# Performance work log

Hardware: AMD Instinct MI355X
Metric: run time of the kernel (lower is better)

Reference implementation:

```python
import jax, jax.numpy as jnp
import numpy as np

B, C, H, W = 4, 256, 64, 64
C8 = C // 8


def setup_inputs() -> dict:
    key = jax.random.key(0)
    ks = jax.random.split(key, 10)
    return {
        "x": jax.random.normal(ks[0], (B, C, H, W), jnp.float32),
        "x_encoder": jax.random.normal(ks[1], (B, C, H, W), jnp.float32),
        "Wq": jax.random.normal(ks[2], (C8, C), jnp.float32) * 0.05,
        "bq": jax.random.normal(ks[3], (C8,), jnp.float32) * 0.05,
        "Wk": jax.random.normal(ks[4], (C8, C), jnp.float32) * 0.05,
        "bk": jax.random.normal(ks[5], (C8,), jnp.float32) * 0.05,
        "Wv": jax.random.normal(ks[6], (C, C), jnp.float32) * 0.05,
        "bv": jax.random.normal(ks[7], (C,), jnp.float32) * 0.05,
        "h_pos": jax.random.normal(ks[8], (1, C8, H, 1), jnp.float32),
        "w_pos": jax.random.normal(ks[9], (1, C8, 1, W), jnp.float32),
        "gamma": jnp.zeros((1,), jnp.float32),
    }


def reference(x, x_encoder, Wq, bq, Wk, bk, Wv, bv, h_pos, w_pos, gamma):
    b, c, h, w = x.shape
    n = h * w
    c8 = Wq.shape[0]
    # 1x1 convs are channel-wise matmuls over flattened spatial dim
    xf = x.reshape(b, c, n)            # [B, C, N]
    xe = x_encoder.reshape(b, c, n)    # [B, C, N]
    q = jnp.einsum("oc,bcn->bno", Wq, xf) + bq[None, None, :]   # [B, N, C8]
    k = jnp.einsum("oc,bcn->bon", Wk, xe) + bk[None, :, None]   # [B, C8, N]
    energy = jnp.einsum("bnc,bcm->bnm", q, k)                    # [B, N, N]
    pos = (h_pos + w_pos).reshape(c8, n)                         # [C8, N]
    energy = energy + jnp.einsum("bnc,cm->bnm", q, pos)
    attn = jax.nn.softmax(energy, axis=-1)                       # [B, N, N]
    v = jnp.einsum("oc,bcn->bon", Wv, xe) + bv[None, :, None]    # [B, C, N]
    out = jnp.einsum("bcm,bnm->bcn", v, attn).reshape(b, c, h, w)
    return gamma * out + x
```

## Files before the change

kernel.cpp:

```cpp
#include <hip/hip_runtime.h>
#include <hip/hip_bf16.h>
#include <math.h>

#define BB 4
#define CC 256
#define C8 32
#define HH 64
#define WW 64
#define NN 4096
#define QBLK 64
#define NT 32
#define LOG2E 1.44269504088896340736f

typedef __attribute__((ext_vector_type(8)))  short bh8;
typedef __attribute__((ext_vector_type(4)))  float f4;
typedef __attribute__((ext_vector_type(16))) float f16v;

#if __has_builtin(__builtin_amdgcn_exp2f)
#define EXP2(x) __builtin_amdgcn_exp2f(x)
#else
#define EXP2(x) exp2f(x)
#endif

static __device__ __forceinline__ unsigned short f2bf(float f) {
    union { float f; unsigned int u; } v; v.f = f;
    return (unsigned short)((v.u + 0x7FFFu + ((v.u >> 16) & 1u)) >> 16);
}

static __device__ __forceinline__ unsigned int cvtpk(float lo, float hi) {
    unsigned int r;
    asm("v_cvt_pk_bf16_f32 %0, %1, %2" : "=v"(r) : "v"(lo), "v"(hi));
    return r;
}

static __device__ __forceinline__ bh8 pack_frag(unsigned int w0, unsigned int w1,
                                                unsigned int w2, unsigned int w3) {
    union { unsigned int u[4]; bh8 v; } z;
    z.u[0] = w0; z.u[1] = w1; z.u[2] = w2; z.u[3] = w3;
    return z.v;
}

__global__ __launch_bounds__(256) void wconv_kernel(
    const float* __restrict__ Wq, const float* __restrict__ Wk,
    const float* __restrict__ Wv, unsigned short* __restrict__ wb)
{
    int f = (blockIdx.x * 256 + threadIdx.x) * 4;
    const float* src;
    if (f < 32 * 256)           src = Wq + f;
    else if (f < 64 * 256)      src = Wk + (f - 32 * 256);
    else                        src = Wv + (f - 64 * 256);
    float4 v = *reinterpret_cast<const float4*>(src);
    ushort4 o;
    o.x = f2bf(v.x); o.y = f2bf(v.y); o.z = f2bf(v.z); o.w = f2bf(v.w);
    *reinterpret_cast<ushort4*>(wb + f) = o;
}

__global__ __launch_bounds__(640, 1) void proj_kernel(
    const float* __restrict__ x, const float* __restrict__ xe,
    const unsigned short* __restrict__ wb,
    const float* __restrict__ bq, const float* __restrict__ bk,
    const float* __restrict__ bv,
    const float* __restrict__ hp, const float* __restrict__ wp,
    unsigned short* __restrict__ qb, unsigned short* __restrict__ kb,
    unsigned short* __restrict__ vv)
{
    const int b  = blockIdx.x & 3;
    const int n0 = (blockIdx.x >> 2) << 6;
    const int t  = threadIdx.x;
    const int w  = t >> 6;
    const int lane = t & 63;
    const int l15 = lane & 15, l4 = lane >> 4;

    __shared__ unsigned short xT[64][256];
    __shared__ unsigned short xeT[64][256];

    bh8 af[2][8];
    {
        const unsigned short* wrow = wb + (size_t)(w * 32 + l15) * 256 + l4 * 8;
        #pragma unroll
        for (int kk = 0; kk < 8; ++kk) {
            af[0][kk] = *reinterpret_cast<const bh8*>(wrow + kk * 32);
            af[1][kk] = *reinterpret_cast<const bh8*>(wrow + 16 * 256 + kk * 32);
        }
    }

    {
        const float* xb  = x  + (size_t)(b * CC) * NN + n0;
        const float* xeb = xe + (size_t)(b * CC) * NN + n0;
        for (int i = t; i < 4096; i += 640) {
            int c = i >> 4, n4 = (i & 15) << 2;
            float4 a = *reinterpret_cast<const float4*>(xb  + (size_t)c * NN + n4);
            float4 e = *reinterpret_cast<const float4*>(xeb + (size_t)c * NN + n4);
            #pragma unroll
            for (int j = 0; j < 4; ++j) {
                int n  = n4 + j;
                int cs = c ^ ((n & 7) << 3);
                xT[n][cs]  = f2bf((&a.x)[j]);
                xeT[n][cs] = f2bf((&e.x)[j]);
            }
        }
    }
    __syncthreads();

    const unsigned short* lds = (w == 0) ? &xT[0][0] : &xeT[0][0];
    f4 acc[2][4] = {};
    #pragma unroll
    for (int kk = 0; kk < 8; ++kk) {
        bh8 bf[4];
        #pragma unroll
        for (int nf = 0; nf < 4; ++nf) {
            int n  = nf * 16 + l15;
            int c0 = (kk * 32 + l4 * 8) ^ ((n & 7) << 3);
            bf[nf] = *reinterpret_cast<const bh8*>(lds + n * 256 + c0);
        }
        #pragma unroll
        for (int nf = 0; nf < 4; ++nf) {
            acc[0][nf] = __builtin_amdgcn_mfma_f32_16x16x32_bf16(af[0][kk], bf[nf], acc[0][nf], 0, 0, 0);
            acc[1][nf] = __builtin_amdgcn_mfma_f32_16x16x32_bf16(af[1][kk], bf[nf], acc[1][nf], 0, 0, 0);
        }
    }

    if (w < 2) {
        unsigned short* dst = (w == 0 ? qb : kb) + (size_t)(b * NN) * C8;
        const float* bias = (w == 0) ? bq : bk;
        #pragma unroll
        for (int mf = 0; mf < 2; ++mf) {
            #pragma unroll
            for (int nf = 0; nf < 4; ++nf) {
                int n  = n0 + nf * 16 + l15;
                int oo = mf * 16 + l4 * 4;
                ushort4 pk;
                #pragma unroll
                for (int r = 0; r < 4; ++r) {
                    int o = oo + r;
                    float val = acc[mf][nf][r] + bias[o];
                    if (w == 1) val += hp[o * HH + (n >> 6)] + wp[o * WW + (n & 63)];
                    else        val *= LOG2E;
                    (&pk.x)[r] = f2bf(val);
                }
                *reinterpret_cast<ushort4*>(dst + (size_t)n * C8 + oo) = pk;
            }
        }
    } else {
        #pragma unroll
        for (int mf = 0; mf < 2; ++mf) {
            int cb = (w - 2) * 32 + mf * 16 + l4 * 4;
            #pragma unroll
            for (int r = 0; r < 4; ++r) {
                float bvv = bv[cb + r];
                #pragma unroll
                for (int nf = 0; nf < 4; ++nf) {
                    int n = n0 + nf * 16 + l15;
                    size_t idx = (((size_t)b * 128 + (n >> 5)) * 256 + cb + r) * 32 + (n & 31);
                    vv[idx] = f2bf(acc[mf][nf][r] + bvv);
                }
            }
        }
    }
}

__global__ __launch_bounds__(512, 1) void attn_flash_kernel(
    const unsigned short* __restrict__ qb, const unsigned short* __restrict__ kb,
    const unsigned short* __restrict__ v,  const float* __restrict__ x,
    const float* __restrict__ gamma, float* __restrict__ out)
{
    const int b    = blockIdx.x & 3;
    const int r0   = (blockIdx.x >> 2) << 6;
    const int t    = threadIdx.x;
    const int w    = t >> 6;
    const int lane = t & 63;
    const int l31  = lane & 31;
    const int h    = lane >> 5;
    const int ks   = w & 3;
    const int cq   = w >> 2;
    const int c0   = cq * 128;

    __shared__ float mO[2][3][64][17];
    __shared__ float mML[2][3][64];

    bh8 qf[2][2];
    #pragma unroll
    for (int qt = 0; qt < 2; ++qt)
        #pragma unroll
        for (int cf = 0; cf < 2; ++cf)
            qf[qt][cf] = *reinterpret_cast<const bh8*>(
                qb + ((size_t)(b * NN) + r0 + qt * 32 + l31) * C8 + cf * 16 + 8 * h);

    const int kb0 = ks * (NN / 4);
    const unsigned short* kp = kb + ((size_t)(b * NN) + kb0 + l31) * C8 + 8 * h;
    const unsigned short* vbase =
        v + (((size_t)b * 128 + ks * 32) * 256 + c0 + l31) * 32 + 8 * h;

    f16v zero16;
    #pragma unroll
    for (int r = 0; r < 16; ++r) zero16[r] = 0.f;

    f16v acc[2][4];
    #pragma unroll
    for (int qt = 0; qt < 2; ++qt)
        #pragma unroll
        for (int ct = 0; ct < 4; ++ct)
            acc[qt][ct] = zero16;

    float l_[2] = { 0.f, 0.f };

    bh8 kf0 = *reinterpret_cast<const bh8*>(kp);
    bh8 kf1 = *reinterpret_cast<const bh8*>(kp + 16);

    for (int tt = 0; tt < NT; ++tt) {
        bh8 vf[4][2];
        {
            const unsigned short* vt = vbase + (size_t)tt * 8192;
            #pragma unroll
            for (int ct = 0; ct < 4; ++ct)
                #pragma unroll
                for (int kk = 0; kk < 2; ++kk)
                    vf[ct][kk] = *reinterpret_cast<const bh8*>(vt + ct * 1024 + kk * 16);
        }
        bh8 nk0, nk1;
        {
            int tn = (tt + 1 < NT) ? tt + 1 : tt;
            const unsigned short* knx = kp + (size_t)tn * 32 * C8;
            nk0 = *reinterpret_cast<const bh8*>(knx);
            nk1 = *reinterpret_cast<const bh8*>(knx + 16);
        }

        #pragma unroll
        for (int qt = 0; qt < 2; ++qt) {
            f16v s = __builtin_amdgcn_mfma_f32_32x32x16_bf16(kf0, qf[qt][0], zero16, 0, 0, 0);
            s = __builtin_amdgcn_mfma_f32_32x32x16_bf16(kf1, qf[qt][1], s, 0, 0, 0);

            #pragma unroll
            for (int r = 0; r < 16; ++r) s[r] = EXP2(s[r]);
            float rs = (((s[0] + s[1]) + (s[2] + s[3])) + ((s[4] + s[5]) + (s[6] + s[7])))
                     + (((s[8] + s[9]) + (s[10] + s[11])) + ((s[12] + s[13]) + (s[14] + s[15])));
            l_[qt] += rs;

            bh8 pf[2];
            #pragma unroll
            for (int kk = 0; kk < 2; ++kk) {
                unsigned int A  = cvtpk(s[8 * kk + 0], s[8 * kk + 1]);
                unsigned int A2 = cvtpk(s[8 * kk + 2], s[8 * kk + 3]);
                unsigned int Bv = cvtpk(s[8 * kk + 4], s[8 * kk + 5]);
                unsigned int B2 = cvtpk(s[8 * kk + 6], s[8 * kk + 7]);
                asm volatile("v_permlane32_swap_b32 %0, %1" : "+v"(Bv), "+v"(A));
                asm volatile("v_permlane32_swap_b32 %0, %1" : "+v"(B2), "+v"(A2));
                pf[kk] = pack_frag(A, A2, Bv, B2);
            }

            #pragma unroll
            for (int ct = 0; ct < 4; ++ct) {
                acc[qt][ct] = __builtin_amdgcn_mfma_f32_32x32x16_bf16(vf[ct][0], pf[0], acc[qt][ct], 0, 0, 0);
                acc[qt][ct] = __builtin_amdgcn_mfma_f32_32x32x16_bf16(vf[ct][1], pf[1], acc[qt][ct], 0, 0, 0);
            }
        }
        kf0 = nk0; kf1 = nk1;
    }

    float lt[2];
    #pragma unroll
    for (int qt = 0; qt < 2; ++qt) {
        float u0 = l_[qt], u1 = l_[qt];
        asm volatile("v_permlane32_swap_b32 %0, %1" : "+v"(u0), "+v"(u1));
        lt[qt] = u0 + u1;
    }

    const float gg = gamma[0];
    #pragma unroll
    for (int qt = 0; qt < 2; ++qt) {
        float Linv = 0.f;
        #pragma unroll
        for (int ct = 0; ct < 4; ++ct) {
            if (ks != 0) {
                #pragma unroll
                for (int rq = 0; rq < 4; ++rq) {
                    f4 tv;
                    tv[0] = acc[qt][ct][rq * 4 + 0];
                    tv[1] = acc[qt][ct][rq * 4 + 1];
                    tv[2] = acc[qt][ct][rq * 4 + 2];
                    tv[3] = acc[qt][ct][rq * 4 + 3];
                    *reinterpret_cast<f4*>(&mO[cq][ks - 1][lane][rq * 4]) = tv;
                }
                if (ct == 0) mML[cq][ks - 1][lane] = lt[qt];
            }
            __syncthreads();
            if (ks == 0) {
                if (ct == 0) {
                    float L = lt[qt] + mML[cq][0][lane] + mML[cq][1][lane] + mML[cq][2][lane];
                    Linv = gg / L;
                }
                #pragma unroll
                for (int r = 0; r < 16; ++r) {
                    float o = acc[qt][ct][r] + mO[cq][0][lane][r]
                            + mO[cq][1][lane][r] + mO[cq][2][lane][r];
                    int c = c0 + ct * 32 + (r & 3) + 8 * (r >> 2) + 4 * h;
                    size_t idx = ((size_t)(b * CC) + c) * NN + r0 + qt * 32 + l31;
                    out[idx] = o * Linv + x[idx];
                }
            }
            __syncthreads();
        }
    }
}

extern "C" void kernel_launch(void* const* d_in, const int* in_sizes, int n_in,
                              void* d_out, int out_size, void* d_ws, size_t ws_size,
                              hipStream_t stream)
{
    (void)in_sizes; (void)n_in; (void)out_size; (void)ws_size;

    const float* x   = (const float*)d_in[0];
    const float* xe  = (const float*)d_in[1];
    const float* Wq  = (const float*)d_in[2];
    const float* bq  = (const float*)d_in[3];
    const float* Wk  = (const float*)d_in[4];
    const float* bk  = (const float*)d_in[5];
    const float* Wv  = (const float*)d_in[6];
    const float* bv  = (const float*)d_in[7];
    const float* hp  = (const float*)d_in[8];
    const float* wp  = (const float*)d_in[9];
    const float* gam = (const float*)d_in[10];
    float* out = (float*)d_out;

    char* ws = (char*)d_ws;
    unsigned short* qb = (unsigned short*)ws;
    unsigned short* kb = (unsigned short*)(ws + (size_t)BB * NN * C8 * 2);
    unsigned short* v  = (unsigned short*)(ws + 2 * (size_t)BB * NN * C8 * 2);
    unsigned short* wbuf = (unsigned short*)(ws + 2 * (size_t)BB * NN * C8 * 2
                                                + (size_t)BB * CC * NN * 2);

    wconv_kernel<<<80, 256, 0, stream>>>(Wq, Wk, Wv, wbuf);
    proj_kernel<<<BB * (NN / 64), 640, 0, stream>>>(x, xe, wbuf, bq, bk, bv, hp, wp, qb, kb, v);
    attn_flash_kernel<<<BB * (NN / QBLK), 512, 0, stream>>>(qb, kb, v, x, gam, out);
}
```

Before: 83.03 us.

## Double-buffer V and K fragments across tiles and raise priority around PV MFMAs

V fragments for the next tile are now prefetched into a ping-pong register buffer along with K, using a macro unrolled by two. The V global-load latency can then overlap the current tile's QK, exp and PV work instead of stalling at the top of each iteration. s_setprio is raised around the PV MFMA block so waves in the MFMA phase get scheduling priority. The extra V buffer adds 8 bh8 registers per thread, which may reduce occupancy or cause spills.

```diff
diff --git a/kernel.cpp b/kernel.cpp
--- a/kernel.cpp
+++ b/kernel.cpp
@@ -204,58 +204,70 @@
 
     float l_[2] = { 0.f, 0.f };
 
-    bh8 kf0 = *reinterpret_cast<const bh8*>(kp);
-    bh8 kf1 = *reinterpret_cast<const bh8*>(kp + 16);
-
-    for (int tt = 0; tt < NT; ++tt) {
-        bh8 vf[4][2];
-        {
-            const unsigned short* vt = vbase + (size_t)tt * 8192;
+    bh8 vfA[4][2], vfB[4][2], kfA[2], kfB[2];
+    {
+        #pragma unroll
+        for (int ct = 0; ct < 4; ++ct)
             #pragma unroll
-            for (int ct = 0; ct < 4; ++ct)
-                #pragma unroll
-                for (int kk = 0; kk < 2; ++kk)
-                    vf[ct][kk] = *reinterpret_cast<const bh8*>(vt + ct * 1024 + kk * 16);
-        }
-        bh8 nk0, nk1;
-        {
-            int tn = (tt + 1 < NT) ? tt + 1 : tt;
-            const unsigned short* knx = kp + (size_t)tn * 32 * C8;
-            nk0 = *reinterpret_cast<const bh8*>(knx);
-            nk1 = *reinterpret_cast<const bh8*>(knx + 16);
-        }
-
-        #pragma unroll
-        for (int qt = 0; qt < 2; ++qt) {
-            f16v s = __builtin_amdgcn_mfma_f32_32x32x16_bf16(kf0, qf[qt][0], zero16, 0, 0, 0);
-            s = __builtin_amdgcn_mfma_f32_32x32x16_bf16(kf1, qf[qt][1], s, 0, 0, 0);
-
-            #pragma unroll
-            for (int r = 0; r < 16; ++r) s[r] = EXP2(s[r]);
-            float rs = (((s[0] + s[1]) + (s[2] + s[3])) + ((s[4] + s[5]) + (s[6] + s[7])))
-                     + (((s[8] + s[9]) + (s[10] + s[11])) + ((s[12] + s[13]) + (s[14] + s[15])));
-            l_[qt] += rs;
-
-            bh8 pf[2];
-            #pragma unroll
-            for (int kk = 0; kk < 2; ++kk) {
-                unsigned int A  = cvtpk(s[8 * kk + 0], s[8 * kk + 1]);
-                unsigned int A2 = cvtpk(s[8 * kk + 2], s[8 * kk + 3]);
-                unsigned int Bv = cvtpk(s[8 * kk + 4], s[8 * kk + 5]);
-                unsigned int B2 = cvtpk(s[8 * kk + 6], s[8 * kk + 7]);
-                asm volatile("v_permlane32_swap_b32 %0, %1" : "+v"(Bv), "+v"(A));
-                asm volatile("v_permlane32_swap_b32 %0, %1" : "+v"(B2), "+v"(A2));
-                pf[kk] = pack_frag(A, A2, Bv, B2);
-            }
-
-            #pragma unroll
-            for (int ct = 0; ct < 4; ++ct) {
-                acc[qt][ct] = __builtin_amdgcn_mfma_f32_32x32x16_bf16(vf[ct][0], pf[0], acc[qt][ct], 0, 0, 0);
-                acc[qt][ct] = __builtin_amdgcn_mfma_f32_32x32x16_bf16(vf[ct][1], pf[1], acc[qt][ct], 0, 0, 0);
-            }
-        }
-        kf0 = nk0; kf1 = nk1;
-    }
+            for (int kk = 0; kk < 2; ++kk)
+                vfA[ct][kk] = *reinterpret_cast<const bh8*>(vbase + ct * 1024 + kk * 16);
+        kfA[0] = *reinterpret_cast<const bh8*>(kp);
+        kfA[1] = *reinterpret_cast<const bh8*>(kp + 16);
+    }
+
+#define ATTN_TILE(VC, VN, KC, KN, TT)                                           \
+    {                                                                           \
+        {     \
+            int tn = ((TT) + 1 < NT) ? (TT) + 1 : (TT);                         \
+            const unsigned short* vt = vbase + (size_t)tn * 8192;               \
+            _Pragma("unroll")                                                   \
+            for (int ct = 0; ct < 4; ++ct)                                      \
+                _Pragma("unroll")                                               \
+                for (int kk = 0; kk < 2; ++kk)                                  \
+                    VN[ct][kk] = *reinterpret_cast<const bh8*>(vt + ct * 1024 + kk * 16); \
+            const unsigned short* knx = kp + (size_t)tn * 32 * C8;              \
+            KN[0] = *reinterpret_cast<const bh8*>(knx);                         \
+            KN[1] = *reinterpret_cast<const bh8*>(knx + 16);                    \
+        }                                                                       \
+        _Pragma("unroll")                                                       \
+        for (int qt = 0; qt < 2; ++qt) {                                        \
+                                \
+            f16v s = __builtin_amdgcn_mfma_f32_32x32x16_bf16(KC[0], qf[qt][0], zero16, 0, 0, 0); \
+            s = __builtin_amdgcn_mfma_f32_32x32x16_bf16(KC[1], qf[qt][1], s, 0, 0, 0); \
+                          \
+            _Pragma("unroll")                                                   \
+            for (int r = 0; r < 16; ++r) s[r] = EXP2(s[r]);                     \
+            float rs = (((s[0] + s[1]) + (s[2] + s[3])) + ((s[4] + s[5]) + (s[6] + s[7]))) \
+                     + (((s[8] + s[9]) + (s[10] + s[11])) + ((s[12] + s[13]) + (s[14] + s[15]))); \
+            l_[qt] += rs;                                                       \
+                           \
+            bh8 pf[2];                                                          \
+            _Pragma("unroll")                                                   \
+            for (int kk = 0; kk < 2; ++kk) {                                    \
+                unsigned int A  = cvtpk(s[8 * kk + 0], s[8 * kk + 1]);          \
+                unsigned int A2 = cvtpk(s[8 * kk + 2], s[8 * kk + 3]);          \
+                unsigned int Bv = cvtpk(s[8 * kk + 4], s[8 * kk + 5]);          \
+                unsigned int B2 = cvtpk(s[8 * kk + 6], s[8 * kk + 7]);          \
+                asm volatile("v_permlane32_swap_b32 %0, %1" : "+v"(Bv), "+v"(A)); \
+                asm volatile("v_permlane32_swap_b32 %0, %1" : "+v"(B2), "+v"(A2)); \
+                pf[kk] = pack_frag(A, A2, Bv, B2);                              \
+            }                                                                   \
+                                              \
+            __builtin_amdgcn_s_setprio(1);                                      \
+            _Pragma("unroll")                                                   \
+            for (int ct = 0; ct < 4; ++ct) {                                    \
+                acc[qt][ct] = __builtin_amdgcn_mfma_f32_32x32x16_bf16(VC[ct][0], pf[0], acc[qt][ct], 0, 0, 0); \
+                acc[qt][ct] = __builtin_amdgcn_mfma_f32_32x32x16_bf16(VC[ct][1], pf[1], acc[qt][ct], 0, 0, 0); \
+            }                                                                   \
+            __builtin_amdgcn_s_setprio(0);                                      \
+        }                                                                       \
+    }
+
+    for (int tt = 0; tt < NT; tt += 2) {
+        ATTN_TILE(vfA, vfB, kfA, kfB, tt);
+        ATTN_TILE(vfB, vfA, kfB, kfA, tt + 1);
+    }
+#undef ATTN_TILE
 
     float lt[2];
     #pragma unroll
```

Result: slower. 283.7 us (+241.7%).
